# Kernel tuning notes

Hardware: AMD Instinct MI355X
Metric: run time of the kernel (lower is better)

Reference implementation:

```python
import jax, jax.numpy as jnp
import numpy as np

EPS2 = 0.01 ** 2   # Plummer softening squared (cfg.v_phi_eps ** 2)
C_STRENGTH = 1.0   # cfg.v_phi_C


def _gelu(x):
    # torch F.gelu default = exact (erf) form
    return jax.nn.gelu(x, approximate=False)


def _pair_dist2(a, b):
    # ||a_t - b_s||^2 via squared-norm expansion; (B,T,d),(B,S,d) -> (B,T,S)
    a2 = jnp.sum(a * a, axis=-1)[:, :, None]
    b2 = jnp.sum(b * b, axis=-1)[:, None, :]
    ab = jnp.einsum('btd,bsd->bts', a, b)
    return jnp.maximum(a2 + b2 - 2.0 * ab, 0.0)


def setup_inputs() -> dict:
    key = jax.random.key(0)
    B, T, d = 8, 512, 128
    dl, K, Hp, Ht = 16, 8, 32, 32
    s = 0.02  # v_phi_init_scale
    ks = jax.random.split(key, 12)
    return {
        'h':        jax.random.normal(ks[0], (B, T, d), dtype=jnp.float32),
        'h_src':    jax.random.normal(ks[1], (B, T, d), dtype=jnp.float32),
        # W_l : Linear(d, dl, bias=False)
        'W_l':      s * jax.random.normal(ks[2], (dl, d), dtype=jnp.float32),
        # W_theta : Linear(d, K, bias=False)
        'W_theta':  s * jax.random.normal(ks[3], (K, d), dtype=jnp.float32),
        # phi_c_net : Linear(1,Hp) -> GELU -> Linear(Hp,1)
        'phi_w1':   s * jax.random.normal(ks[4], (Hp, 1), dtype=jnp.float32),
        'phi_b1':   jnp.zeros((Hp,), dtype=jnp.float32),
        'phi_w2':   s * jax.random.normal(ks[5], (1, Hp), dtype=jnp.float32),
        'phi_b2':   jnp.zeros((1,), dtype=jnp.float32),
        # theta aligner
        'tw_q':     s * jax.random.normal(ks[6], (Ht, K), dtype=jnp.float32),
        'tw_s':     s * jax.random.normal(ks[7], (Ht, K), dtype=jnp.float32),
        'tw_d':     s * jax.random.normal(ks[8], (Ht, K), dtype=jnp.float32),
        'theta_b1': jnp.zeros((Ht,), dtype=jnp.float32),
        'tw2_w':    s * jax.random.normal(ks[9], (1, Ht), dtype=jnp.float32),
        'tw2_b':    jnp.zeros((1,), dtype=jnp.float32),
    }


def reference(h, h_src, W_l, W_theta, phi_w1, phi_b1, phi_w2, phi_b2,
              tw_q, tw_s, tw_d, theta_b1, tw2_w, tw2_b):
    # type / angle projections
    l_q = jnp.einsum('btd,ld->btl', h, W_l)
    l_s = jnp.einsum('btd,ld->btl', h_src, W_l)
    th_q = jnp.einsum('btd,kd->btk', h, W_theta)
    th_s = jnp.einsum('btd,kd->btk', h_src, W_theta)

    # Gaussian gate Phi with learned per-pair inverse bandwidth c
    l_dist2 = _pair_dist2(l_q, l_s)                       # (B,T,T)
    hid = _gelu(l_dist2[..., None] * phi_w1[:, 0] + phi_b1)  # (B,T,T,Hp)
    c = jax.nn.softplus(hid @ phi_w2[0] + phi_b2[0])      # (B,T,T)
    Phi = jnp.exp(-c * l_dist2)

    # bounded value-aligner Theta (low-rank bilinear MLP over pairs)
    proj_t = th_q @ tw_q.T + th_q @ tw_d.T + theta_b1     # (B,T,Ht)
    proj_u = th_s @ tw_s.T - th_s @ tw_d.T                # (B,T,Ht)
    hidden = _gelu(proj_t[:, :, None, :] + proj_u[:, None, :, :])  # (B,T,T,Ht)
    Theta = jnp.tanh(hidden @ tw2_w[0] + tw2_b[0])        # (B,T,T)

    # Plummer-softened 1/r factor
    r = jnp.sqrt(_pair_dist2(h, h_src) + EPS2)
    return -C_STRENGTH * Theta * Phi / r
```

## Files before the change

### kernel.cpp

```cpp
#include <hip/hip_runtime.h>
#include <math.h>

#define T 512
#define EPS2 1e-4f
#define C0G 0.79788456f
#define C1G (-0.13298076f)
#define C2G (0.019947114f)
#define C3G (-0.0023746564f)

typedef __attribute__((ext_vector_type(8))) short s8v;
typedef __attribute__((ext_vector_type(4))) float f4v;

__device__ __forceinline__ uint f2bf(float x){
  uint u = __float_as_uint(x);
  return (u + 0x7FFFu + ((u>>16)&1u)) >> 16;
}
__device__ __forceinline__ uint pk2(float a, float b){ return f2bf(a)|(f2bf(b)<<16); }
__device__ __forceinline__ float bflo(uint u){ return __uint_as_float(u<<16); }
__device__ __forceinline__ float bfhi(uint u){ return __uint_as_float(u & 0xFFFF0000u); }
#define MFMA32 __builtin_amdgcn_mfma_f32_16x16x32_bf16
__device__ __forceinline__ float gf(float x){ float x2=x*x; return x + x2*fmaf(C1G,x2,C0G); }

#define L_HA   0
#define L_UVS  0
#define L_HB   16384
#define L_WB   32768
#define L_UVT  54528
#define L_LPT  67840
#define L_LPS  70912
#define L_K    73984
#define L_TOT  74048

__global__ __launch_bounds__(512,4) void k_all(
    const float* __restrict__ h, const float* __restrict__ hsrc,
    const float* __restrict__ Wl, const float* __restrict__ Wt,
    const float* __restrict__ pw1, const float* __restrict__ pb1,
    const float* __restrict__ pw2, const float* __restrict__ pb2,
    const float* __restrict__ twq, const float* __restrict__ tws,
    const float* __restrict__ twd, const float* __restrict__ tb1,
    const float* __restrict__ tw2, const float* __restrict__ tb2,
    float* __restrict__ out)
{
  __shared__ __align__(16) char smem[L_TOT];
  ushort* hA  = (ushort*)(smem + L_HA);
  ushort* hB  = (ushort*)(smem + L_HB);
  ushort* Wb  = (ushort*)(smem + L_WB);
  ushort* uvT = (ushort*)(smem + L_UVT);
  ushort* uvS = (ushort*)(smem + L_UVS);

  const int tid = threadIdx.x;
  const int Lb  = blockIdx.x;
  const int blk = ((Lb & 7) << 5) | (Lb >> 3);
  const int b   = blk >> 5;
  const int bt  = ((blk >> 2) & 7) * 64;
  const int bs0 = (blk & 3) * 128;
  const int lane = tid & 63, wv = tid >> 6;
  const int hi = lane >> 4, c = lane & 15;
  const int sside = wv >> 2, strip = wv & 3, q0 = sside*2;

  #pragma unroll
  for (int it=0; it<2; ++it){
    const int i = tid + it*512;
    const int row = i >> 4, cid = i & 15;
    const int kk = cid >> 2, h2 = cid & 3;
    const float4* src = (const float4*)(h + (unsigned)(b*T + bt + row)*128u + kk*32 + h2*8);
    const float4 a0 = src[0], a1 = src[1];
    uint4 v; v.x=pk2(a0.x,a0.y); v.y=pk2(a0.z,a0.w); v.z=pk2(a1.x,a1.y); v.w=pk2(a1.z,a1.w);
    *(uint4*)(hA + ((row>>4)*256 + kk*64 + h2*16 + (row&15))*8) = v;
  }
  #pragma unroll
  for (int it=0; it<2; ++it){
    const int i = tid + it*512;
    const int row = i >> 4, cid = i & 15;
    const int kk = cid >> 2, h2 = cid & 3;
    const float4* src = (const float4*)(hsrc + (unsigned)(b*T + bs0 + row)*128u + kk*32 + h2*8);
    const float4 a0 = src[0], a1 = src[1];
    uint4 v; v.x=pk2(a0.x,a0.y); v.y=pk2(a0.z,a0.w); v.z=pk2(a1.x,a1.y); v.w=pk2(a1.z,a1.w);
    *(uint4*)(hB + ((row>>4)*256 + kk*64 + h2*16 + (row&15))*8) = v;
  }
  if (tid < 256){
    const int j = tid>>4, k0 = (tid&15)*8;
    const float4* src = (const float4*)(Wl + j*128 + k0);
    const float4 b0 = src[0], b1 = src[1];
    uint4 v; v.x=pk2(b0.x,b0.y); v.y=pk2(b0.z,b0.w); v.z=pk2(b1.x,b1.y); v.w=pk2(b1.z,b1.w);
    *(uint4*)(Wb + j*136 + k0) = v;
  }
  {
    const int sideF = tid>>8, j=(tid>>3)&31, k0=(tid&7)*16;
    float tw[8];
    #pragma unroll
    for (int m=0;m<8;m++){
      const float d = twd[j*8+m];
      tw[m] = sideF ? (tws[j*8+m]-d) : (twq[j*8+m]+d);
    }
    float o[16];
    #pragma unroll
    for (int i=0;i<16;i++) o[i]=0.f;
    #pragma unroll
    for (int m=0;m<8;m++){
      const float4* wr = (const float4*)(Wt + m*128 + k0);
      #pragma unroll
      for (int g=0; g<4; ++g){
        const float4 qv = wr[g];
        o[g*4+0]=fmaf(tw[m],qv.x,o[g*4+0]); o[g*4+1]=fmaf(tw[m],qv.y,o[g*4+1]);
        o[g*4+2]=fmaf(tw[m],qv.z,o[g*4+2]); o[g*4+3]=fmaf(tw[m],qv.w,o[g*4+3]);
      }
    }
    ushort* dst = Wb + (16 + sideF*32 + j)*136 + k0;
    uint4 v;
    v.x=pk2(o[0],o[1]); v.y=pk2(o[2],o[3]); v.z=pk2(o[4],o[5]); v.w=pk2(o[6],o[7]);
    *(uint4*)dst = v;
    v.x=pk2(o[8],o[9]); v.y=pk2(o[10],o[11]); v.z=pk2(o[12],o[13]); v.w=pk2(o[14],o[15]);
    *(uint4*)(dst+8) = v;
  }
  if (wv == 0){
    const int lj = lane & 31;
    const float kw = (lane < 32) ? (0.5f * pw2[lj]) : 0.f;
    const float bb = pb1[lj], mm = pw1[lj];
    float bp[9], mp[9];
    bp[0]=1.f; mp[0]=1.f;
    #pragma unroll
    for (int i=1;i<9;i++){ bp[i]=bp[i-1]*bb; mp[i]=mp[i-1]*mm; }
    float Kq[9];
    Kq[0] = kw*(bb + C0G*bp[2] + C1G*bp[4] + C2G*bp[6] + C3G*bp[8]);
    Kq[1] = kw*mp[1]*(1.f + 2.f*C0G*bp[1] + 4.f*C1G*bp[3] + 6.f*C2G*bp[5] + 8.f*C3G*bp[7]);
    Kq[2] = kw*mp[2]*(C0G + 6.f*C1G*bp[2] + 15.f*C2G*bp[4] + 28.f*C3G*bp[6]);
    Kq[3] = kw*mp[3]*(4.f*C1G*bp[1] + 20.f*C2G*bp[3] + 56.f*C3G*bp[5]);
    Kq[4] = kw*mp[4]*(C1G + 15.f*C2G*bp[2] + 70.f*C3G*bp[4]);
    Kq[5] = kw*mp[5]*(6.f*C2G*bp[1] + 56.f*C3G*bp[3]);
    Kq[6] = kw*mp[6]*(C2G + 28.f*C3G*bp[2]);
    Kq[7] = kw*mp[7]*(8.f*C3G*bp[1]);
    Kq[8] = kw*mp[8]*C3G;
    #pragma unroll
    for (int m=1;m<64;m<<=1){
      #pragma unroll
      for (int i=0;i<9;i++) Kq[i] += __shfl_xor(Kq[i], m);
    }
    if (lane==0){
      Kq[0] += pb2[0];
      #pragma unroll
      for (int i=0;i<9;i++) ((float*)(smem+L_K))[i] = Kq[i];
    }
  }
  __syncthreads();

  const ushort* myT = sside ? hB : hA;
  f4v p0={0,0,0,0}, p1={0,0,0,0}, p2={0,0,0,0};
  float nrm = 0.f;
  #pragma unroll
  for (int kk=0;kk<4;kk++){
    union { s8v s; uint4 u; } U;
    U.s = *(const s8v*)(myT + (strip*256 + kk*64 + lane)*8);
    { float x;
      x=bflo(U.u.x); nrm=fmaf(x,x,nrm); x=bfhi(U.u.x); nrm=fmaf(x,x,nrm);
      x=bflo(U.u.y); nrm=fmaf(x,x,nrm); x=bfhi(U.u.y); nrm=fmaf(x,x,nrm);
      x=bflo(U.u.z); nrm=fmaf(x,x,nrm); x=bfhi(U.u.z); nrm=fmaf(x,x,nrm);
      x=bflo(U.u.w); nrm=fmaf(x,x,nrm); x=bfhi(U.u.w); nrm=fmaf(x,x,nrm); }
    const int ko = kk*32 + hi*8;
    const s8v bl = *(const s8v*)(Wb + (c)*136 + ko);
    const s8v b0 = *(const s8v*)(Wb + (16 + 32*sside + c)*136 + ko);
    const s8v b1 = *(const s8v*)(Wb + (32 + 32*sside + c)*136 + ko);
    p0 = MFMA32(U.s, b0, p0,0,0,0);
    p1 = MFMA32(U.s, b1, p1,0,0,0);
    p2 = MFMA32(U.s, bl, p2,0,0,0);
  }
  nrm += __shfl_xor(nrm,16); nrm += __shfl_xor(nrm,32);
  s8v ah[4];
  #pragma unroll
  for (int kk=0;kk<4;kk++) ah[kk] = *(const s8v*)(hA + (strip*256 + kk*64 + lane)*8);
  __syncthreads();

  const float w2a = tw2[c], w2b = tw2[c+16];
  const float tb2v = tb2[0];
  {
    const float t1a = sside ? 0.f : tb1[c];
    const float t1b = sside ? 0.f : tb1[c+16];
    ushort* uvMe = sside ? uvS : uvT;
    char* lpBase = smem + (sside ? L_LPS : L_LPT);
    if (hi==0) *(float*)(lpBase + (strip*16 + c)*48 + 32) = nrm;
    #pragma unroll
    for (int r=0;r<4;r++){
      const int row = strip*16 + hi*4 + r;
      const float a0 = p0[r] + t1a, a1 = p1[r] + t1b;
      const float lv = p2[r];
      float pab = fmaf(w2a, gf(a0), w2b*gf(a1));
      float pl  = lv*lv;
      #pragma unroll
      for (int m=1;m<16;m<<=1){ pab += __shfl_xor(pab,m); pl += __shfl_xor(pl,m); }
      if (c==0){
        float* hb_ = (float*)(lpBase + row*48 + 32);
        hb_[1] = pl;
        hb_[2] = sside ? 0.5f*pab : fmaf(0.5f, pab, tb2v);
      }
      ((ushort*)(lpBase))[row*24 + c] = (ushort)f2bf(lv);
      const float a02=a0*a0, a12=a1*a1;
      if (sside){
        uvMe[row*104 +      c] = (ushort)f2bf(a0);      uvMe[row*104 + 16 + c] = (ushort)f2bf(a1);
        uvMe[row*104 + 32 + c] = (ushort)f2bf(a02);     uvMe[row*104 + 48 + c] = (ushort)f2bf(a12);
        uvMe[row*104 + 64 + c] = (ushort)f2bf(a02*a0);  uvMe[row*104 + 80 + c] = (ushort)f2bf(a12*a1);
      } else {
        const float wa0 = w2a*a0, wa1 = w2b*a1;
        uvMe[row*104 +      c] = (ushort)f2bf(wa0*fmaf(2.f*C1G, a02, C0G));
        uvMe[row*104 + 16 + c] = (ushort)f2bf(wa1*fmaf(2.f*C1G, a12, C0G));
        uvMe[row*104 + 32 + c] = (ushort)f2bf(3.f*C1G*w2a*a02);
        uvMe[row*104 + 48 + c] = (ushort)f2bf(3.f*C1G*w2b*a12);
        uvMe[row*104 + 64 + c] = (ushort)f2bf(2.f*C1G*wa0);
        uvMe[row*104 + 80 + c] = (ushort)f2bf(2.f*C1G*wa1);
      }
    }
  }
  __syncthreads();

  float K[9];
  #pragma unroll
  for (int i=0;i<9;i++) K[i] = ((const float*)(smem+L_K))[i];

  #define PAIR_PHASE(BS)                                                        \
  {                                                                             \
    f4v acch[2], accz[2], accl[2];                                              \
    _Pragma("unroll")                                                           \
    for (int qq=0;qq<2;qq++){ acch[qq]=(f4v){0,0,0,0}; accz[qq]=(f4v){0,0,0,0}; accl[qq]=(f4v){0,0,0,0}; } \
    _Pragma("unroll")                                                           \
    for (int kk=0;kk<4;kk++){                                                   \
      _Pragma("unroll")                                                         \
      for (int qq=0;qq<2;qq++)                                                  \
        acch[qq] = MFMA32(ah[kk], *(const s8v*)(hB + ((q0+qq)*256 + kk*64 + lane)*8), acch[qq],0,0,0); \
    }                                                                           \
    _Pragma("unroll")                                                           \
    for (int ks=0;ks<3;ks++){                                                   \
      const s8v au = *(const s8v*)(uvT + (strip*16 + c)*104 + ks*32 + hi*8);    \
      _Pragma("unroll")                                                         \
      for (int qq=0;qq<2;qq++)                                                  \
        accz[qq] = MFMA32(au, *(const s8v*)(uvS + ((q0+qq)*16 + c)*104 + ks*32 + hi*8), accz[qq],0,0,0); \
    }                                                                           \
    {                                                                           \
      union { uint4 u; s8v s; } Z; Z.u = make_uint4(0,0,0,0);                   \
      const s8v al_ = (hi<2) ? *(const s8v*)(smem + L_LPT + (strip*16+c)*48 + hi*16) : Z.s; \
      _Pragma("unroll")                                                         \
      for (int qq=0;qq<2;qq++){                                                 \
        const s8v bq = (hi<2) ? *(const s8v*)(smem + L_LPS + ((q0+qq)*16+c)*48 + hi*16) : Z.s; \
        accl[qq] = MFMA32(al_, bq, accl[qq],0,0,0);                             \
      }                                                                         \
    }                                                                           \
    float h2t[4], l2t[4], alv[4];                                               \
    _Pragma("unroll")                                                           \
    for (int r=0;r<4;r++){                                                      \
      const float* th_ = (const float*)(smem + L_LPT + (strip*16 + hi*4 + r)*48 + 32); \
      h2t[r]=th_[0]; l2t[r]=th_[1]; alv[r]=th_[2];                              \
    }                                                                           \
    _Pragma("unroll")                                                           \
    for (int qq=0;qq<2;qq++){                                                   \
      const int sidx = (q0+qq)*16 + c;                                          \
      const float* sh_ = (const float*)(smem + L_LPS + sidx*48 + 32);           \
      const float h2s=sh_[0], l2s=sh_[1], bet=sh_[2];                           \
      _Pragma("unroll")                                                         \
      for (int r=0;r<4;r++){                                                    \
        const float d2 = fmaxf(fmaf(-2.f, acch[qq][r], h2t[r] + h2s), 0.f);     \
        const float ir = rsqrtf(d2 + EPS2);                                     \
        const float l2 = fmaxf(fmaf(-2.f, accl[qq][r], l2t[r] + l2s), 0.f);     \
        const float lam = fminf(l2, 16.f);                                      \
        float zc = K[8];                                                        \
        _Pragma("unroll")                                                       \
        for (int i=7;i>=0;i--) zc = fmaf(zc, lam, K[i]);                        \
        const float cc  = __logf(1.f + __expf(zc));                             \
        const float phi = __expf(-cc * l2);                                     \
        const float z   = accz[qq][r] + alv[r] + bet;                           \
        const float th  = z * fmaf(z*z, -0.33333334f, 1.f);                     \
        __builtin_nontemporal_store(-th * phi * ir,                             \
          out + (unsigned)(b*T + bt + strip*16 + hi*4 + r)*T + (BS) + sidx);    \
      }                                                                         \
    }                                                                           \
  }

  PAIR_PHASE(bs0)

  __syncthreads();
  #pragma unroll
  for (int it=0; it<2; ++it){
    const int i = tid + it*512;
    const int row = i >> 4, cid = i & 15;
    const int kk = cid >> 2, h2 = cid & 3;
    const float4* src = (const float4*)(hsrc + (unsigned)(b*T + bs0 + 64 + row)*128u + kk*32 + h2*8);
    const float4 a0 = src[0], a1 = src[1];
    uint4 v; v.x=pk2(a0.x,a0.y); v.y=pk2(a0.z,a0.w); v.z=pk2(a1.x,a1.y); v.w=pk2(a1.z,a1.w);
    *(uint4*)(hB + ((row>>4)*256 + kk*64 + h2*16 + (row&15))*8) = v;
  }
  __syncthreads();
  if (sside == 1){
    f4v q0v={0,0,0,0}, q1v={0,0,0,0}, q2v={0,0,0,0};
    float nr2 = 0.f;
    #pragma unroll
    for (int kk=0;kk<4;kk++){
      union { s8v s; uint4 u; } U;
      U.s = *(const s8v*)(hB + (strip*256 + kk*64 + lane)*8);
      { float x;
        x=bflo(U.u.x); nr2=fmaf(x,x,nr2); x=bfhi(U.u.x); nr2=fmaf(x,x,nr2);
        x=bflo(U.u.y); nr2=fmaf(x,x,nr2); x=bfhi(U.u.y); nr2=fmaf(x,x,nr2);
        x=bflo(U.u.z); nr2=fmaf(x,x,nr2); x=bfhi(U.u.z); nr2=fmaf(x,x,nr2);
        x=bflo(U.u.w); nr2=fmaf(x,x,nr2); x=bfhi(U.u.w); nr2=fmaf(x,x,nr2); }
      const int ko = kk*32 + hi*8;
      const s8v bl = *(const s8v*)(Wb + (c)*136 + ko);
      const s8v b0 = *(const s8v*)(Wb + (48 + c)*136 + ko);
      const s8v b1 = *(const s8v*)(Wb + (64 + c)*136 + ko);
      q0v = MFMA32(U.s, b0, q0v,0,0,0);
      q1v = MFMA32(U.s, b1, q1v,0,0,0);
      q2v = MFMA32(U.s, bl, q2v,0,0,0);
    }
    nr2 += __shfl_xor(nr2,16); nr2 += __shfl_xor(nr2,32);
    char* lpBase = smem + L_LPS;
    if (hi==0) *(float*)(lpBase + (strip*16 + c)*48 + 32) = nr2;
    #pragma unroll
    for (int r=0;r<4;r++){
      const int row = strip*16 + hi*4 + r;
      const float a0 = q0v[r], a1 = q1v[r];
      const float lv = q2v[r];
      float pab = fmaf(w2a, gf(a0), w2b*gf(a1));
      float pl  = lv*lv;
      #pragma unroll
      for (int m=1;m<16;m<<=1){ pab += __shfl_xor(pab,m); pl += __shfl_xor(pl,m); }
      if (c==0){
        float* hb_ = (float*)(lpBase + row*48 + 32);
        hb_[1] = pl;
        hb_[2] = 0.5f*pab;
      }
      ((ushort*)(lpBase))[row*24 + c] = (ushort)f2bf(lv);
      const float a02=a0*a0, a12=a1*a1;
      uvS[row*104 +      c] = (ushort)f2bf(a0);      uvS[row*104 + 16 + c] = (ushort)f2bf(a1);
      uvS[row*104 + 32 + c] = (ushort)f2bf(a02);     uvS[row*104 + 48 + c] = (ushort)f2bf(a12);
      uvS[row*104 + 64 + c] = (ushort)f2bf(a02*a0);  uvS[row*104 + 80 + c] = (ushort)f2bf(a12*a1);
    }
  }
  __syncthreads();
  PAIR_PHASE(bs0 + 64)
  #undef PAIR_PHASE
}

extern "C" void kernel_launch(void* const* d_in, const int* in_sizes, int n_in,
                              void* d_out, int out_size, void* d_ws, size_t ws_size,
                              hipStream_t stream) {
  const float* h    = (const float*)d_in[0];
  const float* hsrc = (const float*)d_in[1];
  const float* Wl   = (const float*)d_in[2];
  const float* Wt   = (const float*)d_in[3];
  const float* pw1  = (const float*)d_in[4];
  const float* pb1  = (const float*)d_in[5];
  const float* pw2  = (const float*)d_in[6];
  const float* pb2  = (const float*)d_in[7];
  const float* twq  = (const float*)d_in[8];
  const float* tws  = (const float*)d_in[9];
  const float* twd  = (const float*)d_in[10];
  const float* tb1  = (const float*)d_in[11];
  const float* tw2  = (const float*)d_in[12];
  const float* tb2  = (const float*)d_in[13];
  float* out = (float*)d_out;

  k_all<<<dim3(256,1,1), dim3(512,1,1), 0, stream>>>(
      h,hsrc,Wl,Wt,pw1,pb1,pw2,pb2,twq,tws,twd,tb1,tw2,tb2,out);
}
```

Measured before the change: 20.79 us.

## Load both source tiles upfront and drop mid-kernel reload and syncs

All three input tiles (h and both hsrc halves) are loaded into shared memory at the start, and the projections for all three are done in one phase. The second-half hsrc reload and its two extra barriers between the pair phases go away. The price is about 120 KB of dynamic LDS per block, so launch bounds drop to one block per CU. With 256 blocks on 256 CUs this is probably neutral for occupancy, though latency hiding within a CU may be lower. It also adds a hipFuncSetAttribute call on every launch.

```diff
diff --git a/kernel.cpp b/kernel.cpp
--- a/kernel.cpp
+++ b/kernel.cpp
@@ -22,16 +22,19 @@
 __device__ __forceinline__ float gf(float x){ float x2=x*x; return x + x2*fmaf(C1G,x2,C0G); }
 
 #define L_HA   0
-#define L_UVS  0
-#define L_HB   16384
-#define L_WB   32768
-#define L_UVT  54528
-#define L_LPT  67840
-#define L_LPS  70912
-#define L_K    73984
-#define L_TOT  74048
-
-__global__ __launch_bounds__(512,4) void k_all(
+#define L_HB0  16384
+#define L_HB1  32768
+#define L_WB   49152
+#define L_UVT  70912
+#define L_UVS0 84224
+#define L_UVS1 97536
+#define L_LPT  110848
+#define L_LPS0 113920
+#define L_LPS1 116992
+#define L_K    120064
+#define L_TOT  120128
+
+__global__ __launch_bounds__(512,1) void k_all(
     const float* __restrict__ h, const float* __restrict__ hsrc,
     const float* __restrict__ Wl, const float* __restrict__ Wt,
     const float* __restrict__ pw1, const float* __restrict__ pb1,
@@ -41,12 +44,14 @@
     const float* __restrict__ tw2, const float* __restrict__ tb2,
     float* __restrict__ out)
 {
-  __shared__ __align__(16) char smem[L_TOT];
-  ushort* hA  = (ushort*)(smem + L_HA);
-  ushort* hB  = (ushort*)(smem + L_HB);
-  ushort* Wb  = (ushort*)(smem + L_WB);
-  ushort* uvT = (ushort*)(smem + L_UVT);
-  ushort* uvS = (ushort*)(smem + L_UVS);
+  extern __shared__ __align__(16) char smem[];
+  ushort* hA   = (ushort*)(smem + L_HA);
+  ushort* hB0  = (ushort*)(smem + L_HB0);
+  ushort* hB1  = (ushort*)(smem + L_HB1);
+  ushort* Wb   = (ushort*)(smem + L_WB);
+  ushort* uvT  = (ushort*)(smem + L_UVT);
+  ushort* uvS0 = (ushort*)(smem + L_UVS0);
+  ushort* uvS1 = (ushort*)(smem + L_UVS1);
 
   const int tid = threadIdx.x;
   const int Lb  = blockIdx.x;
@@ -59,24 +64,18 @@
   const int sside = wv >> 2, strip = wv & 3, q0 = sside*2;
 
   #pragma unroll
-  for (int it=0; it<2; ++it){
+  for (int it=0; it<6; ++it){
     const int i = tid + it*512;
-    const int row = i >> 4, cid = i & 15;
+    const int tile = i >> 10, i1 = i & 1023;
+    const int row = i1 >> 4, cid = i1 & 15;
     const int kk = cid >> 2, h2 = cid & 3;
-    const float4* src = (const float4*)(h + (unsigned)(b*T + bt + row)*128u + kk*32 + h2*8);
+    const float* base = (tile==0) ? h + (unsigned)(b*T + bt)*128u
+                                  : hsrc + (unsigned)(b*T + bs0 + (tile==2?64:0))*128u;
+    const float4* src = (const float4*)(base + (unsigned)row*128u + kk*32 + h2*8);
     const float4 a0 = src[0], a1 = src[1];
     uint4 v; v.x=pk2(a0.x,a0.y); v.y=pk2(a0.z,a0.w); v.z=pk2(a1.x,a1.y); v.w=pk2(a1.z,a1.w);
-    *(uint4*)(hA + ((row>>4)*256 + kk*64 + h2*16 + (row&15))*8) = v;
-  }
-  #pragma unroll
-  for (int it=0; it<2; ++it){
-    const int i = tid + it*512;
-    const int row = i >> 4, cid = i & 15;
-    const int kk = cid >> 2, h2 = cid & 3;
-    const float4* src = (const float4*)(hsrc + (unsigned)(b*T + bs0 + row)*128u + kk*32 + h2*8);
-    const float4 a0 = src[0], a1 = src[1];
-    uint4 v; v.x=pk2(a0.x,a0.y); v.y=pk2(a0.z,a0.w); v.z=pk2(a1.x,a1.y); v.w=pk2(a1.z,a1.w);
-    *(uint4*)(hB + ((row>>4)*256 + kk*64 + h2*16 + (row&15))*8) = v;
+    ushort* dst = (tile==0) ? hA : (tile==1 ? hB0 : hB1);
+    *(uint4*)(dst + ((row>>4)*256 + kk*64 + h2*16 + (row&15))*8) = v;
   }
   if (tid < 256){
     const int j = tid>>4, k0 = (tid&15)*8;
@@ -113,7 +112,79 @@
     v.x=pk2(o[8],o[9]); v.y=pk2(o[10],o[11]); v.z=pk2(o[12],o[13]); v.w=pk2(o[14],o[15]);
     *(uint4*)(dst+8) = v;
   }
-  if (wv == 0){
+  __syncthreads();
+
+  const float w2a = tw2[c], w2b = tw2[c+16];
+  const float tb2v = tb2[0];
+
+  #define PROJ_PACK(SRC_TILE, WROW0, IS_T, UVDST, LPOFF)                        \
+  {                                                                             \
+    f4v p0={0,0,0,0}, p1={0,0,0,0}, p2={0,0,0,0};                               \
+    float nrm = 0.f;                                                            \
+    _Pragma("unroll")                                                           \
+    for (int kk=0;kk<4;kk++){                                                   \
+      union { s8v s; uint4 u; } U;                                              \
+      U.s = *(const s8v*)((SRC_TILE) + (strip*256 + kk*64 + lane)*8);           \
+      { float x;                                                                \
+        x=bflo(U.u.x); nrm=fmaf(x,x,nrm); x=bfhi(U.u.x); nrm=fmaf(x,x,nrm);     \
+        x=bflo(U.u.y); nrm=fmaf(x,x,nrm); x=bfhi(U.u.y); nrm=fmaf(x,x,nrm);     \
+        x=bflo(U.u.z); nrm=fmaf(x,x,nrm); x=bfhi(U.u.z); nrm=fmaf(x,x,nrm);     \
+        x=bflo(U.u.w); nrm=fmaf(x,x,nrm); x=bfhi(U.u.w); nrm=fmaf(x,x,nrm); }   \
+      const int ko = kk*32 + hi*8;                                              \
+      const s8v bl = *(const s8v*)(Wb + (c)*136 + ko);                          \
+      const s8v b0 = *(const s8v*)(Wb + ((WROW0) + c)*136 + ko);                \
+      const s8v b1 = *(const s8v*)(Wb + ((WROW0) + 16 + c)*136 + ko);           \
+      p0 = MFMA32(U.s, b0, p0,0,0,0);                                           \
+      p1 = MFMA32(U.s, b1, p1,0,0,0);                                           \
+      p2 = MFMA32(U.s, bl, p2,0,0,0);                                           \
+    }                                                                           \
+    nrm += __shfl_xor(nrm,16); nrm += __shfl_xor(nrm,32);                       \
+    char* lpBase = smem + (LPOFF);                                              \
+    if (hi==0) *(float*)(lpBase + (strip*16 + c)*48 + 32) = nrm;                \
+    _Pragma("unroll")                                                           \
+    for (int r=0;r<4;r++){                                                      \
+      const int row = strip*16 + hi*4 + r;                                      \
+      const float a0 = p0[r] + ((IS_T) ? tb1[c]    : 0.f);                      \
+      const float a1 = p1[r] + ((IS_T) ? tb1[c+16] : 0.f);                      \
+      const float lv = p2[r];                                                   \
+      float pab = fmaf(w2a, gf(a0), w2b*gf(a1));                                \
+      float pl  = lv*lv;                                                        \
+      _Pragma("unroll")                                                         \
+      for (int m=1;m<16;m<<=1){ pab += __shfl_xor(pab,m); pl += __shfl_xor(pl,m); } \
+      if (c==0){                                                                \
+        float* hb_ = (float*)(lpBase + row*48 + 32);                            \
+        hb_[1] = pl;                                                            \
+        hb_[2] = (IS_T) ? fmaf(0.5f, pab, tb2v) : 0.5f*pab;                     \
+      }                                                                         \
+      ((ushort*)(lpBase))[row*24 + c] = (ushort)f2bf(lv);                       \
+      const float a02=a0*a0, a12=a1*a1;                                         \
+      if (IS_T){                                                                \
+        const float wa0 = w2a*a0, wa1 = w2b*a1;                                 \
+        (UVDST)[row*104 +      c] = (ushort)f2bf(wa0*fmaf(2.f*C1G, a02, C0G));  \
+        (UVDST)[row*104 + 16 + c] = (ushort)f2bf(wa1*fmaf(2.f*C1G, a12, C0G));  \
+        (UVDST)[row*104 + 32 + c] = (ushort)f2bf(3.f*C1G*w2a*a02);              \
+        (UVDST)[row*104 + 48 + c] = (ushort)f2bf(3.f*C1G*w2b*a12);              \
+        (UVDST)[row*104 + 64 + c] = (ushort)f2bf(2.f*C1G*wa0);                  \
+        (UVDST)[row*104 + 80 + c] = (ushort)f2bf(2.f*C1G*wa1);                  \
+      } else {                                                                  \
+        (UVDST)[row*104 +      c] = (ushort)f2bf(a0);                           \
+        (UVDST)[row*104 + 16 + c] = (ushort)f2bf(a1);                           \
+        (UVDST)[row*104 + 32 + c] = (ushort)f2bf(a02);                          \
+        (UVDST)[row*104 + 48 + c] = (ushort)f2bf(a12);                          \
+        (UVDST)[row*104 + 64 + c] = (ushort)f2bf(a02*a0);                       \
+        (UVDST)[row*104 + 80 + c] = (ushort)f2bf(a12*a1);                       \
+      }                                                                         \
+    }                                                                           \
+  }
+
+  if (sside == 0){
+    PROJ_PACK(hA, 16, 1, uvT, L_LPT)
+  } else {
+    PROJ_PACK(hB0, 48, 0, uvS0, L_LPS0)
+  }
+  if (sside == 0){
+    PROJ_PACK(hB1, 48, 0, uvS1, L_LPS1)
+  } else if (wv == 4){
     const int lj = lane & 31;
     const float kw = (lane < 32) ? (0.5f * pw2[lj]) : 0.f;
     const float bb = pb1[lj], mm = pw1[lj];
@@ -142,80 +213,17 @@
       for (int i=0;i<9;i++) ((float*)(smem+L_K))[i] = Kq[i];
     }
   }
+  #undef PROJ_PACK
   __syncthreads();
 
-  const ushort* myT = sside ? hB : hA;
-  f4v p0={0,0,0,0}, p1={0,0,0,0}, p2={0,0,0,0};
-  float nrm = 0.f;
+  float K[9];
   #pragma unroll
-  for (int kk=0;kk<4;kk++){
-    union { s8v s; uint4 u; } U;
-    U.s = *(const s8v*)(myT + (strip*256 + kk*64 + lane)*8);
-    { float x;
-      x=bflo(U.u.x); nrm=fmaf(x,x,nrm); x=bfhi(U.u.x); nrm=fmaf(x,x,nrm);
-      x=bflo(U.u.y); nrm=fmaf(x,x,nrm); x=bfhi(U.u.y); nrm=fmaf(x,x,nrm);
-      x=bflo(U.u.z); nrm=fmaf(x,x,nrm); x=bfhi(U.u.z); nrm=fmaf(x,x,nrm);
-      x=bflo(U.u.w); nrm=fmaf(x,x,nrm); x=bfhi(U.u.w); nrm=fmaf(x,x,nrm); }
-    const int ko = kk*32 + hi*8;
-    const s8v bl = *(const s8v*)(Wb + (c)*136 + ko);
-    const s8v b0 = *(const s8v*)(Wb + (16 + 32*sside + c)*136 + ko);
-    const s8v b1 = *(const s8v*)(Wb + (32 + 32*sside + c)*136 + ko);
-    p0 = MFMA32(U.s, b0, p0,0,0,0);
-    p1 = MFMA32(U.s, b1, p1,0,0,0);
-    p2 = MFMA32(U.s, bl, p2,0,0,0);
-  }
-  nrm += __shfl_xor(nrm,16); nrm += __shfl_xor(nrm,32);
+  for (int i=0;i<9;i++) K[i] = ((const float*)(smem+L_K))[i];
   s8v ah[4];
   #pragma unroll
   for (int kk=0;kk<4;kk++) ah[kk] = *(const s8v*)(hA + (strip*256 + kk*64 + lane)*8);
-  __syncthreads();
-
-  const float w2a = tw2[c], w2b = tw2[c+16];
-  const float tb2v = tb2[0];
-  {
-    const float t1a = sside ? 0.f : tb1[c];
-    const float t1b = sside ? 0.f : tb1[c+16];
-    ushort* uvMe = sside ? uvS : uvT;
-    char* lpBase = smem + (sside ? L_LPS : L_LPT);
-    if (hi==0) *(float*)(lpBase + (strip*16 + c)*48 + 32) = nrm;
-    #pragma unroll
-    for (int r=0;r<4;r++){
-      const int row = strip*16 + hi*4 + r;
-      const float a0 = p0[r] + t1a, a1 = p1[r] + t1b;
-      const float lv = p2[r];
-      float pab = fmaf(w2a, gf(a0), w2b*gf(a1));
-      float pl  = lv*lv;
-      #pragma unroll
-      for (int m=1;m<16;m<<=1){ pab += __shfl_xor(pab,m); pl += __shfl_xor(pl,m); }
-      if (c==0){
-        float* hb_ = (float*)(lpBase + row*48 + 32);
-        hb_[1] = pl;
-        hb_[2] = sside ? 0.5f*pab : fmaf(0.5f, pab, tb2v);
-      }
-      ((ushort*)(lpBase))[row*24 + c] = (ushort)f2bf(lv);
-      const float a02=a0*a0, a12=a1*a1;
-      if (sside){
-        uvMe[row*104 +      c] = (ushort)f2bf(a0);      uvMe[row*104 + 16 + c] = (ushort)f2bf(a1);
-        uvMe[row*104 + 32 + c] = (ushort)f2bf(a02);     uvMe[row*104 + 48 + c] = (ushort)f2bf(a12);
-        uvMe[row*104 + 64 + c] = (ushort)f2bf(a02*a0);  uvMe[row*104 + 80 + c] = (ushort)f2bf(a12*a1);
-      } else {
-        const float wa0 = w2a*a0, wa1 = w2b*a1;
-        uvMe[row*104 +      c] = (ushort)f2bf(wa0*fmaf(2.f*C1G, a02, C0G));
-        uvMe[row*104 + 16 + c] = (ushort)f2bf(wa1*fmaf(2.f*C1G, a12, C0G));
-        uvMe[row*104 + 32 + c] = (ushort)f2bf(3.f*C1G*w2a*a02);
-        uvMe[row*104 + 48 + c] = (ushort)f2bf(3.f*C1G*w2b*a12);
-        uvMe[row*104 + 64 + c] = (ushort)f2bf(2.f*C1G*wa0);
-        uvMe[row*104 + 80 + c] = (ushort)f2bf(2.f*C1G*wa1);
-      }
-    }
-  }
-  __syncthreads();
-
-  float K[9];
-  #pragma unroll
-  for (int i=0;i<9;i++) K[i] = ((const float*)(smem+L_K))[i];
-
-  #define PAIR_PHASE(BS)                                                        \
+
+  #define PAIR_PHASE(HBX, UVSX, LPSOFF, BS)                                     \
   {                                                                             \
     f4v acch[2], accz[2], accl[2];                                              \
     _Pragma("unroll")                                                           \
@@ -224,21 +232,21 @@
     for (int kk=0;kk<4;kk++){                                                   \
       _Pragma("unroll")                                                         \
       for (int qq=0;qq<2;qq++)                                                  \
-        acch[qq] = MFMA32(ah[kk], *(const s8v*)(hB + ((q0+qq)*256 + kk*64 + lane)*8), acch[qq],0,0,0); \
+        acch[qq] = MFMA32(ah[kk], *(const s8v*)((HBX) + ((q0+qq)*256 + kk*64 + lane)*8), acch[qq],0,0,0); \
     }                                                                           \
     _Pragma("unroll")                                                           \
     for (int ks=0;ks<3;ks++){                                                   \
       const s8v au = *(const s8v*)(uvT + (strip*16 + c)*104 + ks*32 + hi*8);    \
       _Pragma("unroll")                                                         \
       for (int qq=0;qq<2;qq++)                                                  \
-        accz[qq] = MFMA32(au, *(const s8v*)(uvS + ((q0+qq)*16 + c)*104 + ks*32 + hi*8), accz[qq],0,0,0); \
+        accz[qq] = MFMA32(au, *(const s8v*)((UVSX) + ((q0+qq)*16 + c)*104 + ks*32 + hi*8), accz[qq],0,0,0); \
     }                                                                           \
     {                                                                           \
       union { uint4 u; s8v s; } Z; Z.u = make_uint4(0,0,0,0);                   \
       const s8v al_ = (hi<2) ? *(const s8v*)(smem + L_LPT + (strip*16+c)*48 + hi*16) : Z.s; \
       _Pragma("unroll")                                                         \
       for (int qq=0;qq<2;qq++){                                                 \
-        const s8v bq = (hi<2) ? *(const s8v*)(smem + L_LPS + ((q0+qq)*16+c)*48 + hi*16) : Z.s; \
+        const s8v bq = (hi<2) ? *(const s8v*)(smem + (LPSOFF) + ((q0+qq)*16+c)*48 + hi*16) : Z.s; \
         accl[qq] = MFMA32(al_, bq, accl[qq],0,0,0);                             \
       }                                                                         \
     }                                                                           \
@@ -251,7 +259,7 @@
     _Pragma("unroll")                                                           \
     for (int qq=0;qq<2;qq++){                                                   \
       const int sidx = (q0+qq)*16 + c;                                          \
-      const float* sh_ = (const float*)(smem + L_LPS + sidx*48 + 32);           \
+      const float* sh_ = (const float*)(smem + (LPSOFF) + sidx*48 + 32);        \
       const float h2s=sh_[0], l2s=sh_[1], bet=sh_[2];                           \
       _Pragma("unroll")                                                         \
       for (int r=0;r<4;r++){                                                    \
@@ -272,66 +280,8 @@
     }                                                                           \
   }
 
-  PAIR_PHASE(bs0)
-
-  __syncthreads();
-  #pragma unroll
-  for (int it=0; it<2; ++it){
-    const int i = tid + it*512;
-    const int row = i >> 4, cid = i & 15;
-    const int kk = cid >> 2, h2 = cid & 3;
-    const float4* src = (const float4*)(hsrc + (unsigned)(b*T + bs0 + 64 + row)*128u + kk*32 + h2*8);
-    const float4 a0 = src[0], a1 = src[1];
-    uint4 v; v.x=pk2(a0.x,a0.y); v.y=pk2(a0.z,a0.w); v.z=pk2(a1.x,a1.y); v.w=pk2(a1.z,a1.w);
-    *(uint4*)(hB + ((row>>4)*256 + kk*64 + h2*16 + (row&15))*8) = v;
-  }
-  __syncthreads();
-  if (sside == 1){
-    f4v q0v={0,0,0,0}, q1v={0,0,0,0}, q2v={0,0,0,0};
-    float nr2 = 0.f;
-    #pragma unroll
-    for (int kk=0;kk<4;kk++){
-      union { s8v s; uint4 u; } U;
-      U.s = *(const s8v*)(hB + (strip*256 + kk*64 + lane)*8);
-      { float x;
-        x=bflo(U.u.x); nr2=fmaf(x,x,nr2); x=bfhi(U.u.x); nr2=fmaf(x,x,nr2);
-        x=bflo(U.u.y); nr2=fmaf(x,x,nr2); x=bfhi(U.u.y); nr2=fmaf(x,x,nr2);
-        x=bflo(U.u.z); nr2=fmaf(x,x,nr2); x=bfhi(U.u.z); nr2=fmaf(x,x,nr2);
-        x=bflo(U.u.w); nr2=fmaf(x,x,nr2); x=bfhi(U.u.w); nr2=fmaf(x,x,nr2); }
-      const int ko = kk*32 + hi*8;
-      const s8v bl = *(const s8v*)(Wb + (c)*136 + ko);
-      const s8v b0 = *(const s8v*)(Wb + (48 + c)*136 + ko);
-      const s8v b1 = *(const s8v*)(Wb + (64 + c)*136 + ko);
-      q0v = MFMA32(U.s, b0, q0v,0,0,0);
-      q1v = MFMA32(U.s, b1, q1v,0,0,0);
-      q2v = MFMA32(U.s, bl, q2v,0,0,0);
-    }
-    nr2 += __shfl_xor(nr2,16); nr2 += __shfl_xor(nr2,32);
-    char* lpBase = smem + L_LPS;
-    if (hi==0) *(float*)(lpBase + (strip*16 + c)*48 + 32) = nr2;
-    #pragma unroll
-    for (int r=0;r<4;r++){
-      const int row = strip*16 + hi*4 + r;
-      const float a0 = q0v[r], a1 = q1v[r];
-      const float lv = q2v[r];
-      float pab = fmaf(w2a, gf(a0), w2b*gf(a1));
-      float pl  = lv*lv;
-      #pragma unroll
-      for (int m=1;m<16;m<<=1){ pab += __shfl_xor(pab,m); pl += __shfl_xor(pl,m); }
-      if (c==0){
-        float* hb_ = (float*)(lpBase + row*48 + 32);
-        hb_[1] = pl;
-        hb_[2] = 0.5f*pab;
-      }
-      ((ushort*)(lpBase))[row*24 + c] = (ushort)f2bf(lv);
-      const float a02=a0*a0, a12=a1*a1;
-      uvS[row*104 +      c] = (ushort)f2bf(a0);      uvS[row*104 + 16 + c] = (ushort)f2bf(a1);
-      uvS[row*104 + 32 + c] = (ushort)f2bf(a02);     uvS[row*104 + 48 + c] = (ushort)f2bf(a12);
-      uvS[row*104 + 64 + c] = (ushort)f2bf(a02*a0);  uvS[row*104 + 80 + c] = (ushort)f2bf(a12*a1);
-    }
-  }
-  __syncthreads();
-  PAIR_PHASE(bs0 + 64)
+  PAIR_PHASE(hB0, uvS0, L_LPS0, bs0)
+  PAIR_PHASE(hB1, uvS1, L_LPS1, bs0 + 64)
   #undef PAIR_PHASE
 }
 
@@ -354,6 +304,8 @@
   const float* tb2  = (const float*)d_in[13];
   float* out = (float*)d_out;
 
-  k_all<<<dim3(256,1,1), dim3(512,1,1), 0, stream>>>(
+  hipFuncSetAttribute((const void*)k_all,
+                      hipFuncAttributeMaxDynamicSharedMemorySize, L_TOT);
+  k_all<<<dim3(256,1,1), dim3(512,1,1), L_TOT, stream>>>(
       h,hsrc,Wl,Wt,pw1,pb1,pw2,pb2,twq,tws,twd,tb1,tw2,tb2,out);
 }
```

Measured after the change: 19.28 us. -7.3%, faster.
